# Performance work log

Hardware: AMD Instinct MI355X
Metric: run time of the kernel (lower is better)

Reference implementation:

```python
import jax, jax.numpy as jnp
import numpy as np


def setup_inputs() -> dict:
    n, r, e = 100000, 16, 16
    E = 3200000
    key = jax.random.key(0)
    k1, k2, k3, k4 = jax.random.split(key, 4)
    weights = jax.random.normal(k1, (r, n, e), dtype=jnp.float32) * (np.sqrt(2.0) * np.sqrt(6.0 / (n + e)))
    edge_src = jax.random.randint(k2, (E,), 0, n, dtype=jnp.int32)
    edge_rel = jax.random.randint(k3, (E,), 0, r, dtype=jnp.int32)
    edge_dst = jax.random.randint(k4, (E,), 0, n, dtype=jnp.int32)
    return {"weights": weights, "edge_src": edge_src, "edge_rel": edge_rel, "edge_dst": edge_dst}


def reference(weights, edge_src, edge_rel, edge_dst):
    # weights: (r, n, e). Horizontal adjacency A[i, p*n + j] = 1/deg(i) for edge (i, p, j).
    # h = A @ weights.reshape(r*n, e)  ==  segment-sum over edges of weights[p, j] / deg(i).
    r, n, e = weights.shape
    E = edge_src.shape[0]
    # row sums of the unnormalized adjacency (out-degree across all relations)
    deg = jax.ops.segment_sum(jnp.ones((E,), dtype=weights.dtype), edge_src, num_segments=n)
    vals = 1.0 / jnp.where(deg == 0, 1.0, deg)[edge_src]  # (E,)
    msgs = weights[edge_rel, edge_dst] * vals[:, None]     # (E, e) gather + scale
    h = jax.ops.segment_sum(msgs, edge_src, num_segments=n)  # (n, e)
    return h
```

## Files before the change

### kernel.cpp

```cpp
#include <hip/hip_runtime.h>


static constexpr int EDIM   = 16;
static constexpr int NREL   = 16;
static constexpr int BSH    = 7;
static constexpr int BNODES = 1 << BSH;
static constexpr int MAXNB  = 1024;
static constexpr int EPW    = 8192;
static constexpr int CAP    = 8192;

__global__ void hist_kernel(const int* __restrict__ src, int* __restrict__ cnt, int E) {
    __shared__ int h[MAXNB];
    int t = threadIdx.x;
    for (int i = t; i < MAXNB; i += 256) h[i] = 0;
    __syncthreads();
    int base = blockIdx.x * EPW;
    int end = min(base + EPW, E);
    int nfull = (end - base) >> 2;
    const int4* p4 = (const int4*)(src + base);
    for (int q = t; q < nfull; q += 256) {
        int4 v = p4[q];
        atomicAdd(&h[v.x >> BSH], 1);
        atomicAdd(&h[v.y >> BSH], 1);
        atomicAdd(&h[v.z >> BSH], 1);
        atomicAdd(&h[v.w >> BSH], 1);
    }
    for (int k = base + (nfull << 2) + t; k < end; k += 256) atomicAdd(&h[src[k] >> BSH], 1);
    __syncthreads();
    for (int i = t; i < MAXNB; i += 256) {
        int c = h[i];
        if (c) atomicAdd(&cnt[i], c);
    }
}

__global__ void scan_kernel(const int* __restrict__ cnt, int* __restrict__ off,
                            int* __restrict__ cursor, int nb) {
    __shared__ int s[1024];
    int t = threadIdx.x;
    int v = (t < nb) ? cnt[t] : 0;
    s[t] = v;
    __syncthreads();
    int acc = v;
    for (int d = 1; d < 1024; d <<= 1) {
        int x = (t >= d) ? s[t - d] : 0;
        __syncthreads();
        acc += x;
        s[t] = acc;
        __syncthreads();
    }
    if (t < nb) { off[t] = acc - v; cursor[t] = acc - v; }
    if (t == 1023) off[nb] = acc;
}

__global__ void split_kernel(const int* __restrict__ src, const int* __restrict__ rel,
                             const int* __restrict__ dst, int* __restrict__ cursor,
                             unsigned* __restrict__ recs, int E) {
    __shared__ int h[MAXNB];
    int t = threadIdx.x;
    for (int i = t; i < MAXNB; i += 256) h[i] = 0;
    __syncthreads();
    int base = blockIdx.x * EPW;
    int end = min(base + EPW, E);
    int nfull = (end - base) >> 2;
    const int4* s4 = (const int4*)(src + base);
    for (int q = t; q < nfull; q += 256) {
        int4 v = s4[q];
        atomicAdd(&h[v.x >> BSH], 1);
        atomicAdd(&h[v.y >> BSH], 1);
        atomicAdd(&h[v.z >> BSH], 1);
        atomicAdd(&h[v.w >> BSH], 1);
    }
    for (int k = base + (nfull << 2) + t; k < end; k += 256) atomicAdd(&h[src[k] >> BSH], 1);
    __syncthreads();
    for (int i = t; i < MAXNB; i += 256) {
        int c = h[i];
        h[i] = c ? atomicAdd(&cursor[i], c) : 0;
    }
    __syncthreads();
    const int4* r4 = (const int4*)(rel + base);
    const int4* d4 = (const int4*)(dst + base);
    for (int q = t; q < nfull; q += 256) {
        int4 vs = s4[q], vr = r4[q], vd = d4[q];
        int pos;
        pos = atomicAdd(&h[vs.x >> BSH], 1);
        recs[pos] = ((unsigned)(vs.x & (BNODES - 1)) << 21) | ((unsigned)vr.x << 17) | (unsigned)vd.x;
        pos = atomicAdd(&h[vs.y >> BSH], 1);
        recs[pos] = ((unsigned)(vs.y & (BNODES - 1)) << 21) | ((unsigned)vr.y << 17) | (unsigned)vd.y;
        pos = atomicAdd(&h[vs.z >> BSH], 1);
        recs[pos] = ((unsigned)(vs.z & (BNODES - 1)) << 21) | ((unsigned)vr.z << 17) | (unsigned)vd.z;
        pos = atomicAdd(&h[vs.w >> BSH], 1);
        recs[pos] = ((unsigned)(vs.w & (BNODES - 1)) << 21) | ((unsigned)vr.w << 17) | (unsigned)vd.w;
    }
    for (int k = base + (nfull << 2) + t; k < end; k += 256) {
        int s = src[k];
        int pos = atomicAdd(&h[s >> BSH], 1);
        recs[pos] = ((unsigned)(s & (BNODES - 1)) << 21) | ((unsigned)rel[k] << 17) | (unsigned)dst[k];
    }
}

__global__ __launch_bounds__(512)
void accum_kernel(const float* __restrict__ w, const int* __restrict__ off,
                  const unsigned* __restrict__ recs, float* __restrict__ out,
                  int n) {
    __shared__ unsigned srt[CAP];
    __shared__ int noff[BNODES + 1];
    __shared__ int ncur[BNODES];
    int b = blockIdx.x;
    int t = threadIdx.x;
    int g = t >> 4;
    int l = t & 15;

    int s0 = off[b], s1 = off[b + 1];

    float f[4] = {0.f, 0.f, 0.f, 0.f};
    int   d[4] = {0, 0, 0, 0};

    for (int cbase = s0; cbase < s1; cbase += CAP) {
        int cnt = min(CAP, s1 - cbase);

        if (t < BNODES) ncur[t] = 0;
        __syncthreads();
        for (int i = t; i < cnt; i += 512)
            atomicAdd(&ncur[recs[cbase + i] >> 21], 1);
        __syncthreads();
        if (t < 64) {
            int c0 = ncur[2 * t], c1 = ncur[2 * t + 1];
            int v = c0 + c1;
            for (int dd = 1; dd < 64; dd <<= 1) {
                int x = __shfl_up(v, dd);
                if (t >= dd) v += x;
            }
            int excl = v - (c0 + c1);
            noff[2 * t] = excl;          ncur[2 * t] = excl;
            noff[2 * t + 1] = excl + c0; ncur[2 * t + 1] = excl + c0;
            if (t == 63) noff[BNODES] = v;
        }
        __syncthreads();
        for (int i = t; i < cnt; i += 512) {
            unsigned rc = recs[cbase + i];
            int pos = atomicAdd(&ncur[rc >> 21], 1);
            srt[pos] = rc;
        }
        __syncthreads();

#pragma unroll
        for (int q = 0; q < 4; ++q) {
            int ln = g + (q << 5);
            int a = noff[ln], e = noff[ln + 1];
            d[q] += e - a;
            float fs = 0.f;
            int i = a;
            for (; i + 3 < e; i += 4) {
                unsigned r0 = srt[i], r1 = srt[i + 1], r2 = srt[i + 2], r3 = srt[i + 3];
                int j0 = (int)((r0 >> 17) & 15u) * n + (int)(r0 & 0x1FFFFu);
                int j1 = (int)((r1 >> 17) & 15u) * n + (int)(r1 & 0x1FFFFu);
                int j2 = (int)((r2 >> 17) & 15u) * n + (int)(r2 & 0x1FFFFu);
                int j3 = (int)((r3 >> 17) & 15u) * n + (int)(r3 & 0x1FFFFu);
                float v0 = w[((size_t)j0 << 4) + l];
                float v1 = w[((size_t)j1 << 4) + l];
                float v2 = w[((size_t)j2 << 4) + l];
                float v3 = w[((size_t)j3 << 4) + l];
                fs += (v0 + v1) + (v2 + v3);
            }
            for (; i < e; ++i) {
                unsigned rc = srt[i];
                int j = (int)((rc >> 17) & 15u) * n + (int)(rc & 0x1FFFFu);
                fs += w[((size_t)j << 4) + l];
            }
            f[q] += fs;
        }
        __syncthreads();
    }

#pragma unroll
    for (int q = 0; q < 4; ++q) {
        int ln = g + (q << 5);
        int node = (b << BSH) + ln;
        if (node < n) {
            float inv = d[q] ? 1.0f / (float)d[q] : 0.0f;
            out[(size_t)node * EDIM + l] = f[q] * inv;
        }
    }
}

__global__ void deg_kernel_f(const int* __restrict__ src, float* __restrict__ deg, int E) {
    int k = blockIdx.x * blockDim.x + threadIdx.x;
    if (k < E) atomicAdd(&deg[src[k]], 1.0f);
}
__global__ void scatter_kernel_f(const float* __restrict__ w, const int* __restrict__ src,
                                 const int* __restrict__ rel, const int* __restrict__ dst,
                                 const float* __restrict__ deg, float* __restrict__ out,
                                 int E, int n) {
    long long tid = (long long)blockIdx.x * blockDim.x + threadIdx.x;
    int lane = (int)(tid & 15);
    int k = (int)(tid >> 4);
    if (k >= E) return;
    int s = src[k], p = rel[k], j = dst[k];
    atomicAdd(&out[(size_t)s * EDIM + lane],
              w[((size_t)p * n + j) * EDIM + lane] / deg[s]);
}

extern "C" void kernel_launch(void* const* d_in, const int* in_sizes, int n_in,
                              void* d_out, int out_size, void* d_ws, size_t ws_size,
                              hipStream_t stream) {
    const float* w   = (const float*)d_in[0];
    const int*   src = (const int*)d_in[1];
    const int*   rel = (const int*)d_in[2];
    const int*   dst = (const int*)d_in[3];
    float* out = (float*)d_out;

    int E = in_sizes[1];
    int n = in_sizes[0] / (NREL * EDIM);
    int nb = (n + BNODES - 1) >> BSH;

    size_t need = ((size_t)(3 * MAXNB + 1) + (size_t)E) * sizeof(int);

    if (nb > MAXNB || n >= (1 << 17) || ws_size < need) {
        float* deg = (float*)d_ws;
        hipMemsetAsync(deg, 0, (size_t)n * sizeof(float), stream);
        hipMemsetAsync(out, 0, (size_t)out_size * sizeof(float), stream);
        deg_kernel_f<<<(E + 255) / 256, 256, 0, stream>>>(src, deg, E);
        long long total = (long long)E * EDIM;
        scatter_kernel_f<<<(int)((total + 255) / 256), 256, 0, stream>>>(w, src, rel, dst, deg, out, E, n);
        return;
    }

    int* cnt    = (int*)d_ws;
    int* off    = cnt + MAXNB;
    int* cursor = off + (MAXNB + 1);
    unsigned* recs = (unsigned*)(cursor + MAXNB);

    hipMemsetAsync(cnt, 0, (size_t)MAXNB * sizeof(int), stream);

    int ewgs = (E + EPW - 1) / EPW;
    hist_kernel <<<ewgs, 256, 0, stream>>>(src, cnt, E);
    scan_kernel <<<1, 1024, 0, stream>>>(cnt, off, cursor, nb);
    split_kernel<<<ewgs, 256, 0, stream>>>(src, rel, dst, cursor, recs, E);
    accum_kernel<<<nb, 512, 0, stream>>>(w, off, recs, out, n);
}
```

Measured before the change: 137.1 us.

## Split accum bucket across two blocks and enlarge hist/split work per block

```diff
diff --git a/kernel.cpp b/kernel.cpp
--- a/kernel.cpp
+++ b/kernel.cpp
@@ -6,28 +6,28 @@
 static constexpr int BSH    = 7;
 static constexpr int BNODES = 1 << BSH;
 static constexpr int MAXNB  = 1024;
-static constexpr int EPW    = 8192;
-static constexpr int CAP    = 8192;
+static constexpr int EPW    = 16384;
+static constexpr int CAP    = 4096;
 
 __global__ void hist_kernel(const int* __restrict__ src, int* __restrict__ cnt, int E) {
     __shared__ int h[MAXNB];
     int t = threadIdx.x;
-    for (int i = t; i < MAXNB; i += 256) h[i] = 0;
+    for (int i = t; i < MAXNB; i += 512) h[i] = 0;
     __syncthreads();
     int base = blockIdx.x * EPW;
     int end = min(base + EPW, E);
     int nfull = (end - base) >> 2;
     const int4* p4 = (const int4*)(src + base);
-    for (int q = t; q < nfull; q += 256) {
+    for (int q = t; q < nfull; q += 512) {
         int4 v = p4[q];
         atomicAdd(&h[v.x >> BSH], 1);
         atomicAdd(&h[v.y >> BSH], 1);
         atomicAdd(&h[v.z >> BSH], 1);
         atomicAdd(&h[v.w >> BSH], 1);
     }
-    for (int k = base + (nfull << 2) + t; k < end; k += 256) atomicAdd(&h[src[k] >> BSH], 1);
-    __syncthreads();
-    for (int i = t; i < MAXNB; i += 256) {
+    for (int k = base + (nfull << 2) + t; k < end; k += 512) atomicAdd(&h[src[k] >> BSH], 1);
+    __syncthreads();
+    for (int i = t; i < MAXNB; i += 512) {
         int c = h[i];
         if (c) atomicAdd(&cnt[i], c);
     }
@@ -57,29 +57,29 @@
                              unsigned* __restrict__ recs, int E) {
     __shared__ int h[MAXNB];
     int t = threadIdx.x;
-    for (int i = t; i < MAXNB; i += 256) h[i] = 0;
+    for (int i = t; i < MAXNB; i += 512) h[i] = 0;
     __syncthreads();
     int base = blockIdx.x * EPW;
     int end = min(base + EPW, E);
     int nfull = (end - base) >> 2;
     const int4* s4 = (const int4*)(src + base);
-    for (int q = t; q < nfull; q += 256) {
+    for (int q = t; q < nfull; q += 512) {
         int4 v = s4[q];
         atomicAdd(&h[v.x >> BSH], 1);
         atomicAdd(&h[v.y >> BSH], 1);
         atomicAdd(&h[v.z >> BSH], 1);
         atomicAdd(&h[v.w >> BSH], 1);
     }
-    for (int k = base + (nfull << 2) + t; k < end; k += 256) atomicAdd(&h[src[k] >> BSH], 1);
-    __syncthreads();
-    for (int i = t; i < MAXNB; i += 256) {
+    for (int k = base + (nfull << 2) + t; k < end; k += 512) atomicAdd(&h[src[k] >> BSH], 1);
+    __syncthreads();
+    for (int i = t; i < MAXNB; i += 512) {
         int c = h[i];
         h[i] = c ? atomicAdd(&cursor[i], c) : 0;
     }
     __syncthreads();
     const int4* r4 = (const int4*)(rel + base);
     const int4* d4 = (const int4*)(dst + base);
-    for (int q = t; q < nfull; q += 256) {
+    for (int q = t; q < nfull; q += 512) {
         int4 vs = s4[q], vr = r4[q], vd = d4[q];
         int pos;
         pos = atomicAdd(&h[vs.x >> BSH], 1);
@@ -91,21 +91,22 @@
         pos = atomicAdd(&h[vs.w >> BSH], 1);
         recs[pos] = ((unsigned)(vs.w & (BNODES - 1)) << 21) | ((unsigned)vr.w << 17) | (unsigned)vd.w;
     }
-    for (int k = base + (nfull << 2) + t; k < end; k += 256) {
+    for (int k = base + (nfull << 2) + t; k < end; k += 512) {
         int s = src[k];
         int pos = atomicAdd(&h[s >> BSH], 1);
         recs[pos] = ((unsigned)(s & (BNODES - 1)) << 21) | ((unsigned)rel[k] << 17) | (unsigned)dst[k];
     }
 }
 
-__global__ __launch_bounds__(512)
+__global__ __launch_bounds__(256, 8)
 void accum_kernel(const float* __restrict__ w, const int* __restrict__ off,
                   const unsigned* __restrict__ recs, float* __restrict__ out,
                   int n) {
     __shared__ unsigned srt[CAP];
-    __shared__ int noff[BNODES + 1];
-    __shared__ int ncur[BNODES];
-    int b = blockIdx.x;
+    __shared__ int noff[65];
+    __shared__ int ncur[64];
+    int b    = blockIdx.x >> 1;
+    int half = blockIdx.x & 1;
     int t = threadIdx.x;
     int g = t >> 4;
     int l = t & 15;
@@ -118,49 +119,62 @@
     for (int cbase = s0; cbase < s1; cbase += CAP) {
         int cnt = min(CAP, s1 - cbase);
 
-        if (t < BNODES) ncur[t] = 0;
-        __syncthreads();
-        for (int i = t; i < cnt; i += 512)
-            atomicAdd(&ncur[recs[cbase + i] >> 21], 1);
+        if (t < 64) ncur[t] = 0;
+        __syncthreads();
+        for (int i = t; i < cnt; i += 256) {
+            int ln = (int)(recs[cbase + i] >> 21);
+            if ((ln >> 6) == half) atomicAdd(&ncur[ln & 63], 1);
+        }
         __syncthreads();
         if (t < 64) {
-            int c0 = ncur[2 * t], c1 = ncur[2 * t + 1];
-            int v = c0 + c1;
+            int c = ncur[t];
+            int v = c;
             for (int dd = 1; dd < 64; dd <<= 1) {
                 int x = __shfl_up(v, dd);
                 if (t >= dd) v += x;
             }
-            int excl = v - (c0 + c1);
-            noff[2 * t] = excl;          ncur[2 * t] = excl;
-            noff[2 * t + 1] = excl + c0; ncur[2 * t + 1] = excl + c0;
-            if (t == 63) noff[BNODES] = v;
-        }
-        __syncthreads();
-        for (int i = t; i < cnt; i += 512) {
+            noff[t] = v - c;
+            ncur[t] = v - c;
+            if (t == 63) noff[64] = v;
+        }
+        __syncthreads();
+        for (int i = t; i < cnt; i += 256) {
             unsigned rc = recs[cbase + i];
-            int pos = atomicAdd(&ncur[rc >> 21], 1);
-            srt[pos] = rc;
+            int ln = (int)(rc >> 21);
+            if ((ln >> 6) == half) {
+                int pos = atomicAdd(&ncur[ln & 63], 1);
+                srt[pos] = rc;
+            }
         }
         __syncthreads();
 
 #pragma unroll
         for (int q = 0; q < 4; ++q) {
-            int ln = g + (q << 5);
+            int ln = g + (q << 4);
             int a = noff[ln], e = noff[ln + 1];
             d[q] += e - a;
             float fs = 0.f;
             int i = a;
-            for (; i + 3 < e; i += 4) {
-                unsigned r0 = srt[i], r1 = srt[i + 1], r2 = srt[i + 2], r3 = srt[i + 3];
+            for (; i + 7 < e; i += 8) {
+                unsigned r0 = srt[i],     r1 = srt[i + 1], r2 = srt[i + 2], r3 = srt[i + 3];
+                unsigned r4 = srt[i + 4], r5 = srt[i + 5], r6 = srt[i + 6], r7 = srt[i + 7];
                 int j0 = (int)((r0 >> 17) & 15u) * n + (int)(r0 & 0x1FFFFu);
                 int j1 = (int)((r1 >> 17) & 15u) * n + (int)(r1 & 0x1FFFFu);
                 int j2 = (int)((r2 >> 17) & 15u) * n + (int)(r2 & 0x1FFFFu);
                 int j3 = (int)((r3 >> 17) & 15u) * n + (int)(r3 & 0x1FFFFu);
+                int j4 = (int)((r4 >> 17) & 15u) * n + (int)(r4 & 0x1FFFFu);
+                int j5 = (int)((r5 >> 17) & 15u) * n + (int)(r5 & 0x1FFFFu);
+                int j6 = (int)((r6 >> 17) & 15u) * n + (int)(r6 & 0x1FFFFu);
+                int j7 = (int)((r7 >> 17) & 15u) * n + (int)(r7 & 0x1FFFFu);
                 float v0 = w[((size_t)j0 << 4) + l];
                 float v1 = w[((size_t)j1 << 4) + l];
                 float v2 = w[((size_t)j2 << 4) + l];
                 float v3 = w[((size_t)j3 << 4) + l];
-                fs += (v0 + v1) + (v2 + v3);
+                float v4 = w[((size_t)j4 << 4) + l];
+                float v5 = w[((size_t)j5 << 4) + l];
+                float v6 = w[((size_t)j6 << 4) + l];
+                float v7 = w[((size_t)j7 << 4) + l];
+                fs += ((v0 + v1) + (v2 + v3)) + ((v4 + v5) + (v6 + v7));
             }
             for (; i < e; ++i) {
                 unsigned rc = srt[i];
@@ -174,8 +188,7 @@
 
 #pragma unroll
     for (int q = 0; q < 4; ++q) {
-        int ln = g + (q << 5);
-        int node = (b << BSH) + ln;
+        int node = (b << BSH) + (half << 6) + g + (q << 4);
         if (node < n) {
             float inv = d[q] ? 1.0f / (float)d[q] : 0.0f;
             out[(size_t)node * EDIM + l] = f[q] * inv;
@@ -233,8 +246,8 @@
     hipMemsetAsync(cnt, 0, (size_t)MAXNB * sizeof(int), stream);
 
     int ewgs = (E + EPW - 1) / EPW;
-    hist_kernel <<<ewgs, 256, 0, stream>>>(src, cnt, E);
+    hist_kernel <<<ewgs, 512, 0, stream>>>(src, cnt, E);
     scan_kernel <<<1, 1024, 0, stream>>>(cnt, off, cursor, nb);
-    split_kernel<<<ewgs, 256, 0, stream>>>(src, rel, dst, cursor, recs, E);
-    accum_kernel<<<nb, 512, 0, stream>>>(w, off, recs, out, n);
-}
+    split_kernel<<<ewgs, 512, 0, stream>>>(src, rel, dst, cursor, recs, E);
+    accum_kernel<<<nb * 2, 256, 0, stream>>>(w, off, recs, out, n);
+}
```

Result: faster. 125.5 us (-8.5%).
